# Kernel tuning notes

Measured on AMD Instinct MI355X. Metric: run time of the kernel, lower is better.

The kernel has to match this reference:

```python
import jax, jax.numpy as jnp
import numpy as np

D_MODEL = 1024
D_FF = 1024
NUM_EXPERTS = 8
TOP_K = 2


def setup_inputs() -> dict:
    key = jax.random.key(0)
    ks = jax.random.split(key, 5)
    s_in = 1.0 / np.sqrt(D_MODEL)
    s_ff = 1.0 / np.sqrt(D_FF)
    return {
        "x": jax.random.normal(ks[0], (4, 2048, D_MODEL), dtype=jnp.float32),
        "gate_w": jax.random.normal(ks[1], (NUM_EXPERTS, D_MODEL), dtype=jnp.float32) * s_in,
        # torch Linear weight layout: [out_features, in_features], stacked over experts
        "w_gate": jax.random.normal(ks[2], (NUM_EXPERTS, D_FF, D_MODEL), dtype=jnp.float32) * s_in,
        "w_up": jax.random.normal(ks[3], (NUM_EXPERTS, D_FF, D_MODEL), dtype=jnp.float32) * s_in,
        "w_down": jax.random.normal(ks[4], (NUM_EXPERTS, D_MODEL, D_FF), dtype=jnp.float32) * s_ff,
    }


def reference(x, gate_w, w_gate, w_up, w_down):
    B, S, D = x.shape
    T = B * S
    E = gate_w.shape[0]
    xt = x.reshape(T, D)

    # Router
    logits = xt @ gate_w.T                      # [T, E]
    probs = jax.nn.softmax(logits, axis=-1)
    top_v, top_i = jax.lax.top_k(probs, TOP_K)  # [T, K]
    top_v = top_v / jnp.sum(top_v, axis=-1, keepdims=True)

    tokens_per_expert = jnp.sum(jax.nn.one_hot(top_i, E, dtype=jnp.float32), axis=(0, 1))  # [E]
    f = tokens_per_expert / jnp.sum(tokens_per_expert)
    P = jnp.mean(probs, axis=0)
    aux_loss = E * jnp.sum(f * P)

    # Combine weights: per-token weight for each expert (sum over top-k slots)
    combine = jnp.zeros((T, E), dtype=x.dtype).at[jnp.arange(T)[:, None], top_i].add(top_v)  # [T, E]

    # Dense per-expert SwiGLU (equivalent math to masked gather/scatter loop)
    g = jnp.einsum('td,efd->etf', xt, w_gate)   # [E, T, F]
    u = jnp.einsum('td,efd->etf', xt, w_up)     # [E, T, F]
    act = jax.nn.silu(g) * u
    eo = jnp.einsum('etf,edf->etd', act, w_down)  # [E, T, D]

    out = jnp.einsum('te,etd->td', combine, eo).reshape(B, S, D)
    return out, aux_loss, tokens_per_expert
```

## Files before the change

kernel.cpp:

```cpp
#include <hip/hip_runtime.h>


#define T_TOK   8192
#define DM      1024
#define DFF     1024
#define NE      8
#define TOTS    (2 * T_TOK)
#define R1_BLK  2048
#define CVT_BLK 2048

typedef __attribute__((ext_vector_type(8))) short bf16x8;
typedef __attribute__((ext_vector_type(4))) float f32x4;

#define ASYNC16(gp, lp) __builtin_amdgcn_global_load_lds( \
    (const __attribute__((address_space(1))) unsigned int*)(gp), \
    (__attribute__((address_space(3))) unsigned int*)(lp), 16, 0, 0)

__device__ __forceinline__ unsigned short f2bf(float f) {
    union { float f; unsigned u; } c; c.f = f;
    unsigned r = c.u + 0x7fffu + ((c.u >> 16) & 1u);
    return (unsigned short)(r >> 16);
}
__device__ __forceinline__ float bf2f(unsigned short h) {
    union { unsigned u; float f; } c; c.u = ((unsigned)h) << 16;
    return c.f;
}

__global__ __launch_bounds__(256) void pre_kernel(
    const float* __restrict__ x, const float* __restrict__ gate_w,
    const float* __restrict__ s0, const float* __restrict__ s1, const float* __restrict__ s2,
    unsigned short* __restrict__ d0, unsigned short* __restrict__ d1, unsigned short* __restrict__ d2,
    unsigned short* __restrict__ xb,
    int* __restrict__ topi, float2* __restrict__ topw, float* __restrict__ psum_part)
{
    int tid = threadIdx.x;
    int sub = blockIdx.x >> 1;

    if (blockIdx.x & 1) {
        int base = sub * 256 + tid;
        #pragma unroll
        for (int it = 0; it < 12; ++it) {
            int idx = base + it * (CVT_BLK * 256);
            int seg = idx >> 21;
            int off = (idx & ((1 << 21) - 1)) * 4;
            const float* s = (seg == 0) ? s0 : (seg == 1) ? s1 : s2;
            unsigned short* d = (seg == 0) ? d0 : (seg == 1) ? d1 : d2;
            float4 v = *(const float4*)(s + off);
            ushort4 o;
            o.x = f2bf(v.x); o.y = f2bf(v.y); o.z = f2bf(v.z); o.w = f2bf(v.w);
            *(ushort4*)(d + off) = o;
        }
        return;
    }

    __shared__ float gw[NE * DM];
    __shared__ float blk_psum[NE];

    for (int i = tid; i < NE * DM; i += 256) gw[i] = gate_w[i];
    if (tid < NE) blk_psum[tid] = 0.f;
    __syncthreads();

    int wv = tid >> 6, lane = tid & 63;
    int t = sub * 4 + wv;

    float acc[NE];
    #pragma unroll
    for (int e = 0; e < NE; ++e) acc[e] = 0.f;
    const float* xr = x + (size_t)t * DM;
    unsigned short* xbr = xb + (size_t)t * DM;
    #pragma unroll 4
    for (int i = 0; i < DM / 64; ++i) {
        float xv = xr[i * 64 + lane];
        xbr[i * 64 + lane] = f2bf(xv);
        #pragma unroll
        for (int e = 0; e < NE; ++e)
            acc[e] += xv * gw[e * DM + i * 64 + lane];
    }
    #pragma unroll
    for (int e = 0; e < NE; ++e) {
        float v = acc[e];
        #pragma unroll
        for (int s = 32; s > 0; s >>= 1) v += __shfl_xor(v, s, 64);
        acc[e] = v;
    }
    if (lane == 0) {
        float mx = acc[0];
        #pragma unroll
        for (int e = 1; e < NE; ++e) mx = fmaxf(mx, acc[e]);
        float p[NE], sum = 0.f;
        #pragma unroll
        for (int e = 0; e < NE; ++e) { p[e] = expf(acc[e] - mx); sum += p[e]; }
        float inv = 1.f / sum;
        #pragma unroll
        for (int e = 0; e < NE; ++e) { p[e] *= inv; atomicAdd(&blk_psum[e], p[e]); }
        int i1 = 0; float v1 = p[0];
        #pragma unroll
        for (int e = 1; e < NE; ++e) if (p[e] > v1) { v1 = p[e]; i1 = e; }
        int i2 = -1; float v2 = -1.f;
        #pragma unroll
        for (int e = 0; e < NE; ++e) { if (e == i1) continue; if (p[e] > v2) { v2 = p[e]; i2 = e; } }
        float winv = 1.f / (v1 + v2);
        topi[t] = i1 | (i2 << 8);
        topw[t] = make_float2(v1 * winv, v2 * winv);
    }
    __syncthreads();
    if (tid < NE) psum_part[sub * NE + tid] = blk_psum[tid];
}

__global__ __launch_bounds__(256) void scatfin_kernel(
    const int* __restrict__ topi, const float* __restrict__ psum_part,
    int* __restrict__ elist, int2* __restrict__ cidx,
    int* __restrict__ ecnt, int* __restrict__ ebaseg, float* __restrict__ out_tail)
{
    __shared__ int c8[256 * NE];
    __shared__ int sm[256];
    __shared__ int ebase_sh[NE + 1];
    __shared__ float f8[256 * NE];

    int e = blockIdx.x;
    int tid = threadIdx.x;

    int cnt8[NE];
    #pragma unroll
    for (int j = 0; j < NE; ++j) cnt8[j] = 0;
    #pragma unroll 4
    for (int k = 0; k < 32; ++k) {
        int pk = topi[tid * 32 + k];
        cnt8[pk & 0xff]++;
        cnt8[(pk >> 8) & 0xff]++;
    }
    #pragma unroll
    for (int j = 0; j < NE; ++j) c8[tid * NE + j] = cnt8[j];
    sm[tid] = cnt8[e];
    __syncthreads();

    for (int s = 128; s > 0; s >>= 1) {
        if (tid < s) {
            #pragma unroll
            for (int j = 0; j < NE; ++j)
                c8[tid * NE + j] += c8[(tid + s) * NE + j];
        }
        __syncthreads();
    }
    if (tid == 0) {
        int s = 0;
        for (int j = 0; j < NE; ++j) { ebase_sh[j] = s; s += c8[j]; }
        ebase_sh[NE] = s;
    }
    int mymatch = cnt8[e];
    __syncthreads();
    for (int s = 1; s < 256; s <<= 1) {
        int v = (tid >= s) ? sm[tid - s] : 0;
        __syncthreads();
        sm[tid] += v;
        __syncthreads();
    }
    int wbase = ebase_sh[e] + sm[tid] - mymatch;

    for (int k = 0; k < 32; ++k) {
        int tt = tid * 32 + k;
        int pk = topi[tt];
        int e1 = pk & 0xff, e2 = (pk >> 8) & 0xff;
        if (e1 == e) {
            elist[wbase] = tt;
            ((int*)cidx)[2 * tt] = wbase;
            wbase++;
        } else if (e2 == e) {
            elist[wbase] = tt;
            ((int*)cidx)[2 * tt + 1] = wbase;
            wbase++;
        }
    }
    if (tid == 0) {
        ecnt[e]   = c8[e];
        ebaseg[e] = ebase_sh[e];
    }

    if (e == 0) {
        float s8[NE];
        #pragma unroll
        for (int j = 0; j < NE; ++j) s8[j] = 0.f;
        for (int b = tid; b < R1_BLK; b += 256) {
            const float* row = psum_part + (size_t)b * NE;
            #pragma unroll
            for (int j = 0; j < NE; ++j) s8[j] += row[j];
        }
        #pragma unroll
        for (int j = 0; j < NE; ++j) f8[tid * NE + j] = s8[j];
        __syncthreads();
        for (int s = 128; s > 0; s >>= 1) {
            if (tid < s) {
                #pragma unroll
                for (int j = 0; j < NE; ++j)
                    f8[tid * NE + j] += f8[(tid + s) * NE + j];
            }
            __syncthreads();
        }
        if (tid == 0) {
            float aux = 0.f;
            for (int j = 0; j < NE; ++j) {
                float P = f8[j] / (float)T_TOK;
                float f = (float)c8[j] / (float)(2 * T_TOK);
                aux += f * P;
                out_tail[1 + j] = (float)c8[j];
            }
            out_tail[0] = (float)NE * aux;
        }
    }
}

__global__ __launch_bounds__(256) void gemm1_kernel(
    const unsigned short* __restrict__ xb,
    const unsigned short* __restrict__ wgb,
    const unsigned short* __restrict__ wub,
    const int* __restrict__ elist, const int* __restrict__ ecnt,
    const int* __restrict__ ebaseg,
    unsigned short* __restrict__ Hbuf)
{
    int e = blockIdx.z, mt = blockIdx.y, ft = blockIdx.x;
    int ne = ecnt[e];
    if (mt * 128 >= ne) return;
    int base = ebaseg[e];

    __shared__ unsigned short As[128 * 64];
    __shared__ unsigned short Gs[64 * 64];
    __shared__ unsigned short Us[64 * 64];
    __shared__ int tok[128];

    int tid = threadIdx.x;
    if (tid < 128) {
        int slot = base + mt * 128 + tid;
        tok[tid] = elist[min(slot, TOTS - 1)];
    }
    __syncthreads();

    int wave = tid >> 6, lane = tid & 63;
    int quad = lane >> 4, col = lane & 15;
    int cr = tid >> 3;
    int cl = ((tid & 7) ^ (cr & 7)) * 8;

    const size_t woff = (size_t)e * (size_t)DFF * DM;
    const unsigned short* ap[4];
    #pragma unroll
    for (int j = 0; j < 4; ++j) ap[j] = xb + (size_t)tok[j * 32 + cr] * DM + cl;
    const unsigned short* gp[2];
    const unsigned short* up[2];
    #pragma unroll
    for (int j = 0; j < 2; ++j) {
        gp[j] = wgb + woff + (size_t)(ft * 64 + j * 32 + cr) * DM + cl;
        up[j] = wub + woff + (size_t)(ft * 64 + j * 32 + cr) * DM + cl;
    }
    unsigned short* lA = As + wave * 512;
    unsigned short* lG = Gs + wave * 512;
    unsigned short* lU = Us + wave * 512;

    f32x4 accG[2][4], accU[2][4];
    #pragma unroll
    for (int i = 0; i < 2; ++i)
        #pragma unroll
        for (int n = 0; n < 4; ++n) { accG[i][n] = (f32x4){0,0,0,0}; accU[i][n] = (f32x4){0,0,0,0}; }

    for (int k0 = 0; k0 < DM; k0 += 64) {
        __syncthreads();
        #pragma unroll
        for (int j = 0; j < 4; ++j) ASYNC16(ap[j] + k0, lA + j * 2048);
        #pragma unroll
        for (int j = 0; j < 2; ++j) {
            ASYNC16(gp[j] + k0, lG + j * 2048);
            ASYNC16(up[j] + k0, lU + j * 2048);
        }
        __syncthreads();
        #pragma unroll
        for (int ksoff = 0; ksoff < 8; ksoff += 4) {
            bf16x8 a[2], g[4], u[4];
            #pragma unroll
            for (int i = 0; i < 2; ++i) {
                int m = wave * 32 + i * 16 + col;
                a[i] = *(const bf16x8*)&As[m * 64 + ((quad + ksoff) ^ (m & 7)) * 8];
            }
            #pragma unroll
            for (int n = 0; n < 4; ++n) {
                int nb = n * 16 + col;
                int off = nb * 64 + ((quad + ksoff) ^ (nb & 7)) * 8;
                g[n] = *(const bf16x8*)&Gs[off];
                u[n] = *(const bf16x8*)&Us[off];
            }
            #pragma unroll
            for (int i = 0; i < 2; ++i)
                #pragma unroll
                for (int n = 0; n < 4; ++n) {
                    accG[i][n] = __builtin_amdgcn_mfma_f32_16x16x32_bf16(a[i], g[n], accG[i][n], 0, 0, 0);
                    accU[i][n] = __builtin_amdgcn_mfma_f32_16x16x32_bf16(a[i], u[n], accU[i][n], 0, 0, 0);
                }
        }
    }
    #pragma unroll
    for (int i = 0; i < 2; ++i) {
        #pragma unroll
        for (int r = 0; r < 4; ++r) {
            int pos = mt * 128 + wave * 32 + i * 16 + quad * 4 + r;
            if (pos >= ne) continue;
            unsigned short* hr = Hbuf + (size_t)(base + pos) * DFF + ft * 64 + col;
            #pragma unroll
            for (int n = 0; n < 4; ++n) {
                float gg = accG[i][n][r], uu = accU[i][n][r];
                float h = (gg / (1.f + expf(-gg))) * uu;
                hr[n * 16] = f2bf(h);
            }
        }
    }
}

__global__ __launch_bounds__(256) void gemm2_kernel(
    const unsigned short* __restrict__ Hbuf,
    const unsigned short* __restrict__ wdb,
    const int* __restrict__ ecnt, const int* __restrict__ ebaseg,
    unsigned short* __restrict__ eo)
{
    int e = blockIdx.z, mt = blockIdx.y, dt = blockIdx.x;
    int ne = ecnt[e];
    if (mt * 128 >= ne) return;
    int base = ebaseg[e];

    __shared__ unsigned short As[128 * 64];
    __shared__ unsigned short Bs[128 * 64];

    int tid = threadIdx.x;
    int wave = tid >> 6, lane = tid & 63;
    int quad = lane >> 4, col = lane & 15;
    int wr = (wave >> 1) * 64, wc = (wave & 1) * 64;
    int cr = tid >> 3;
    int cl = ((tid & 7) ^ (cr & 7)) * 8;

    const size_t woff = (size_t)e * (size_t)DM * DFF;
    const unsigned short* ap[4];
    const unsigned short* bp[4];
    #pragma unroll
    for (int j = 0; j < 4; ++j) {
        int hrow = min(base + mt * 128 + j * 32 + cr, TOTS - 1);
        ap[j] = Hbuf + (size_t)hrow * DFF + cl;
        bp[j] = wdb + woff + (size_t)(dt * 128 + j * 32 + cr) * DFF + cl;
    }
    unsigned short* lA = As + wave * 512;
    unsigned short* lB = Bs + wave * 512;

    f32x4 acc[4][4];
    #pragma unroll
    for (int i = 0; i < 4; ++i)
        #pragma unroll
        for (int n = 0; n < 4; ++n) acc[i][n] = (f32x4){0,0,0,0};

    for (int k0 = 0; k0 < DFF; k0 += 64) {
        __syncthreads();
        #pragma unroll
        for (int j = 0; j < 4; ++j) {
            ASYNC16(ap[j] + k0, lA + j * 2048);
            ASYNC16(bp[j] + k0, lB + j * 2048);
        }
        __syncthreads();
        #pragma unroll
        for (int ksoff = 0; ksoff < 8; ksoff += 4) {
            bf16x8 a[4], b[4];
            #pragma unroll
            for (int i = 0; i < 4; ++i) {
                int m = wr + i * 16 + col;
                a[i] = *(const bf16x8*)&As[m * 64 + ((quad + ksoff) ^ (m & 7)) * 8];
            }
            #pragma unroll
            for (int n = 0; n < 4; ++n) {
                int nb = wc + n * 16 + col;
                b[n] = *(const bf16x8*)&Bs[nb * 64 + ((quad + ksoff) ^ (nb & 7)) * 8];
            }
            #pragma unroll
            for (int i = 0; i < 4; ++i)
                #pragma unroll
                for (int n = 0; n < 4; ++n)
                    acc[i][n] = __builtin_amdgcn_mfma_f32_16x16x32_bf16(a[i], b[n], acc[i][n], 0, 0, 0);
        }
    }
    #pragma unroll
    for (int i = 0; i < 4; ++i) {
        #pragma unroll
        for (int r = 0; r < 4; ++r) {
            int pos = mt * 128 + wr + i * 16 + quad * 4 + r;
            if (pos >= ne) continue;
            unsigned short* er = eo + (size_t)(base + pos) * DM + dt * 128 + wc + col;
            #pragma unroll
            for (int n = 0; n < 4; ++n)
                er[n * 16] = f2bf(acc[i][n][r]);
        }
    }
}

__global__ __launch_bounds__(256) void combine_kernel(
    const unsigned short* __restrict__ eo, const float2* __restrict__ topw,
    const int2* __restrict__ cidx, float* __restrict__ out)
{
    int idx = blockIdx.x * 256 + threadIdx.x;
    int t = idx >> 7;
    int c = (idx & 127) << 3;
    float2 w = topw[t];
    int2 rr = cidx[t];
    const unsigned short* p0 = eo + (size_t)rr.x * DM + c;
    const unsigned short* p1 = eo + (size_t)rr.y * DM + c;
    ushort4 a0 = *(const ushort4*)p0;
    ushort4 a1 = *(const ushort4*)(p0 + 4);
    ushort4 b0 = *(const ushort4*)p1;
    ushort4 b1 = *(const ushort4*)(p1 + 4);
    float* orow = out + (size_t)t * DM + c;
    float4 o0, o1;
    o0.x = w.x * bf2f(a0.x) + w.y * bf2f(b0.x);
    o0.y = w.x * bf2f(a0.y) + w.y * bf2f(b0.y);
    o0.z = w.x * bf2f(a0.z) + w.y * bf2f(b0.z);
    o0.w = w.x * bf2f(a0.w) + w.y * bf2f(b0.w);
    o1.x = w.x * bf2f(a1.x) + w.y * bf2f(b1.x);
    o1.y = w.x * bf2f(a1.y) + w.y * bf2f(b1.y);
    o1.z = w.x * bf2f(a1.z) + w.y * bf2f(b1.z);
    o1.w = w.x * bf2f(a1.w) + w.y * bf2f(b1.w);
    *(float4*)orow = o0;
    *(float4*)(orow + 4) = o1;
}

extern "C" void kernel_launch(void* const* d_in, const int* in_sizes, int n_in,
                              void* d_out, int out_size, void* d_ws, size_t ws_size,
                              hipStream_t stream) {
    const float* x      = (const float*)d_in[0];
    const float* gate_w = (const float*)d_in[1];
    const float* w_gate = (const float*)d_in[2];
    const float* w_up   = (const float*)d_in[3];
    const float* w_down = (const float*)d_in[4];
    float* out = (float*)d_out;

    char* p = (char*)d_ws;
    unsigned short* xb   = (unsigned short*)p; p += (size_t)T_TOK * DM * 2;
    unsigned short* wgb  = (unsigned short*)p; p += (size_t)NE * DFF * DM * 2;
    unsigned short* wub  = (unsigned short*)p; p += (size_t)NE * DFF * DM * 2;
    unsigned short* wdb  = (unsigned short*)p; p += (size_t)NE * DM * DFF * 2;
    unsigned short* Hbuf = (unsigned short*)p; p += (size_t)TOTS * DFF * 2;
    int*   elist = (int*)p;   p += (size_t)TOTS * 4;
    int*   ecnt  = (int*)p;   p += NE * 4;
    int*   ebaseg= (int*)p;   p += NE * 4;
    int*   topi  = (int*)p;   p += (size_t)T_TOK * 4;
    float2* topw = (float2*)p; p += (size_t)T_TOK * 8;
    int2*  cidx  = (int2*)p;  p += (size_t)T_TOK * 8;
    float* psum_part = (float*)p; p += (size_t)R1_BLK * NE * 4;
    unsigned short* eo = wgb;

    pre_kernel<<<R1_BLK + CVT_BLK, 256, 0, stream>>>(
        x, gate_w, w_gate, w_up, w_down, wgb, wub, wdb,
        xb, topi, topw, psum_part);
    scatfin_kernel<<<NE, 256, 0, stream>>>(topi, psum_part, elist, cidx, ecnt, ebaseg,
                                           out + (size_t)T_TOK * DM);
    gemm1_kernel<<<dim3(DFF / 64, TOTS / 128, NE), 256, 0, stream>>>(
        xb, wgb, wub, elist, ecnt, ebaseg, Hbuf);
    gemm2_kernel<<<dim3(DM / 128, TOTS / 128, NE), 256, 0, stream>>>(
        Hbuf, wdb, ecnt, ebaseg, eo);
    combine_kernel<<<T_TOK * DM / 8 / 256, 256, 0, stream>>>(eo, topw, cidx, out);
}
```

Before: 336.8 us.

## Fuse combine into down-projection epilogue via weighted atomic scatter-add

```diff
diff --git a/kernel.cpp b/kernel.cpp
--- a/kernel.cpp
+++ b/kernel.cpp
@@ -8,6 +8,7 @@
 #define TOTS    (2 * T_TOK)
 #define R1_BLK  2048
 #define CVT_BLK 2048
+#define ZERO_BLK 1024
 
 typedef __attribute__((ext_vector_type(8))) short bf16x8;
 typedef __attribute__((ext_vector_type(4))) float f32x4;
@@ -108,17 +109,30 @@
 }
 
 __global__ __launch_bounds__(256) void scatfin_kernel(
-    const int* __restrict__ topi, const float* __restrict__ psum_part,
-    int* __restrict__ elist, int2* __restrict__ cidx,
-    int* __restrict__ ecnt, int* __restrict__ ebaseg, float* __restrict__ out_tail)
+    const int* __restrict__ topi, const float2* __restrict__ topw,
+    const float* __restrict__ psum_part,
+    int* __restrict__ elist, float* __restrict__ sw,
+    int* __restrict__ ecnt, int* __restrict__ ebaseg,
+    float* __restrict__ out, float* __restrict__ out_tail)
 {
+    int tid = threadIdx.x;
+
+    if (blockIdx.x >= NE) {
+        int idx = (blockIdx.x - NE) * 256 + tid;
+        #pragma unroll
+        for (int it = 0; it < 8; ++it) {
+            int off = (idx + it * (ZERO_BLK * 256)) * 4;
+            *(float4*)(out + off) = (float4){0.f, 0.f, 0.f, 0.f};
+        }
+        return;
+    }
+
     __shared__ int c8[256 * NE];
     __shared__ int sm[256];
     __shared__ int ebase_sh[NE + 1];
     __shared__ float f8[256 * NE];
 
     int e = blockIdx.x;
-    int tid = threadIdx.x;
 
     int cnt8[NE];
     #pragma unroll
@@ -163,11 +177,11 @@
         int e1 = pk & 0xff, e2 = (pk >> 8) & 0xff;
         if (e1 == e) {
             elist[wbase] = tt;
-            ((int*)cidx)[2 * tt] = wbase;
+            sw[wbase] = topw[tt].x;
             wbase++;
         } else if (e2 == e) {
             elist[wbase] = tt;
-            ((int*)cidx)[2 * tt + 1] = wbase;
+            sw[wbase] = topw[tt].y;
             wbase++;
         }
     }
@@ -314,8 +328,9 @@
 __global__ __launch_bounds__(256) void gemm2_kernel(
     const unsigned short* __restrict__ Hbuf,
     const unsigned short* __restrict__ wdb,
+    const int* __restrict__ elist, const float* __restrict__ sw,
     const int* __restrict__ ecnt, const int* __restrict__ ebaseg,
-    unsigned short* __restrict__ eo)
+    float* __restrict__ out)
 {
     int e = blockIdx.z, mt = blockIdx.y, dt = blockIdx.x;
     int ne = ecnt[e];
@@ -324,8 +339,16 @@
 
     __shared__ unsigned short As[128 * 64];
     __shared__ unsigned short Bs[128 * 64];
+    __shared__ int   stok[128];
+    __shared__ float swt[128];
 
     int tid = threadIdx.x;
+    if (tid < 128) {
+        int slot = min(base + mt * 128 + tid, TOTS - 1);
+        stok[tid] = elist[slot];
+        swt[tid]  = sw[slot];
+    }
+
     int wave = tid >> 6, lane = tid & 63;
     int quad = lane >> 4, col = lane & 15;
     int wr = (wave >> 1) * 64, wc = (wave & 1) * 64;
@@ -382,43 +405,17 @@
     for (int i = 0; i < 4; ++i) {
         #pragma unroll
         for (int r = 0; r < 4; ++r) {
-            int pos = mt * 128 + wr + i * 16 + quad * 4 + r;
+            int local = wr + i * 16 + quad * 4 + r;
+            int pos = mt * 128 + local;
             if (pos >= ne) continue;
-            unsigned short* er = eo + (size_t)(base + pos) * DM + dt * 128 + wc + col;
+            int   t = stok[local];
+            float w = swt[local];
+            float* orow = out + (size_t)t * DM + dt * 128 + wc + col;
             #pragma unroll
             for (int n = 0; n < 4; ++n)
-                er[n * 16] = f2bf(acc[i][n][r]);
-        }
-    }
-}
-
-__global__ __launch_bounds__(256) void combine_kernel(
-    const unsigned short* __restrict__ eo, const float2* __restrict__ topw,
-    const int2* __restrict__ cidx, float* __restrict__ out)
-{
-    int idx = blockIdx.x * 256 + threadIdx.x;
-    int t = idx >> 7;
-    int c = (idx & 127) << 3;
-    float2 w = topw[t];
-    int2 rr = cidx[t];
-    const unsigned short* p0 = eo + (size_t)rr.x * DM + c;
-    const unsigned short* p1 = eo + (size_t)rr.y * DM + c;
-    ushort4 a0 = *(const ushort4*)p0;
-    ushort4 a1 = *(const ushort4*)(p0 + 4);
-    ushort4 b0 = *(const ushort4*)p1;
-    ushort4 b1 = *(const ushort4*)(p1 + 4);
-    float* orow = out + (size_t)t * DM + c;
-    float4 o0, o1;
-    o0.x = w.x * bf2f(a0.x) + w.y * bf2f(b0.x);
-    o0.y = w.x * bf2f(a0.y) + w.y * bf2f(b0.y);
-    o0.z = w.x * bf2f(a0.z) + w.y * bf2f(b0.z);
-    o0.w = w.x * bf2f(a0.w) + w.y * bf2f(b0.w);
-    o1.x = w.x * bf2f(a1.x) + w.y * bf2f(b1.x);
-    o1.y = w.x * bf2f(a1.y) + w.y * bf2f(b1.y);
-    o1.z = w.x * bf2f(a1.z) + w.y * bf2f(b1.z);
-    o1.w = w.x * bf2f(a1.w) + w.y * bf2f(b1.w);
-    *(float4*)orow = o0;
-    *(float4*)(orow + 4) = o1;
+                atomicAdd(&orow[n * 16], w * acc[i][n][r]);
+        }
+    }
 }
 
 extern "C" void kernel_launch(void* const* d_in, const int* in_sizes, int n_in,
@@ -438,22 +435,21 @@
     unsigned short* wdb  = (unsigned short*)p; p += (size_t)NE * DM * DFF * 2;
     unsigned short* Hbuf = (unsigned short*)p; p += (size_t)TOTS * DFF * 2;
     int*   elist = (int*)p;   p += (size_t)TOTS * 4;
+    float* sw    = (float*)p; p += (size_t)TOTS * 4;
     int*   ecnt  = (int*)p;   p += NE * 4;
     int*   ebaseg= (int*)p;   p += NE * 4;
     int*   topi  = (int*)p;   p += (size_t)T_TOK * 4;
     float2* topw = (float2*)p; p += (size_t)T_TOK * 8;
-    int2*  cidx  = (int2*)p;  p += (size_t)T_TOK * 8;
     float* psum_part = (float*)p; p += (size_t)R1_BLK * NE * 4;
-    unsigned short* eo = wgb;
 
     pre_kernel<<<R1_BLK + CVT_BLK, 256, 0, stream>>>(
         x, gate_w, w_gate, w_up, w_down, wgb, wub, wdb,
         xb, topi, topw, psum_part);
-    scatfin_kernel<<<NE, 256, 0, stream>>>(topi, psum_part, elist, cidx, ecnt, ebaseg,
-                                           out + (size_t)T_TOK * DM);
+    scatfin_kernel<<<NE + ZERO_BLK, 256, 0, stream>>>(
+        topi, topw, psum_part, elist, sw, ecnt, ebaseg,
+        out, out + (size_t)T_TOK * DM);
     gemm1_kernel<<<dim3(DFF / 64, TOTS / 128, NE), 256, 0, stream>>>(
         xb, wgb, wub, elist, ecnt, ebaseg, Hbuf);
     gemm2_kernel<<<dim3(DM / 128, TOTS / 128, NE), 256, 0, stream>>>(
-        Hbuf, wdb, ecnt, ebaseg, eo);
-    combine_kernel<<<T_TOK * DM / 8 / 256, 256, 0, stream>>>(eo, topw, cidx, out);
-}
+        Hbuf, wdb, elist, sw, ecnt, ebaseg, out);
+}
```

Result: slower. 365.5 us (+8.5%).
